# Optimization experiments

Hardware: AMD Instinct MI355X
Metric: run time of the kernel (lower is better)

The kernel has to match this reference:

```python
import jax, jax.numpy as jnp
import numpy as np

B, IN_DIM, OUT_DIM, DEGREE = 512, 256, 256, 5
SCALE = 0.5 / (DEGREE + 1)


def setup_inputs() -> dict:
    key = jax.random.key(0)
    k1, k2, k3 = jax.random.split(key, 3)
    x = jax.random.normal(k1, (B, IN_DIM), dtype=jnp.float32)
    slopes = jnp.arange(DEGREE + 1, dtype=jnp.float32)
    weights_p = jax.random.normal(k2, (IN_DIM, OUT_DIM, DEGREE + 1), dtype=jnp.float32) * SCALE
    weights_q = jax.random.normal(k3, (IN_DIM, OUT_DIM, DEGREE + 1), dtype=jnp.float32) * SCALE
    return {"x": x, "slopes": slopes, "weights_p": weights_p, "weights_q": weights_q}


def reference(x, slopes, weights_p, weights_q):
    # Training-mode forward (temp = 1.0): logsumexp over degree axis.
    # lin: (B, in_dim, 1, degree+1)
    lin = x[:, :, None, None] * slopes
    # broadcast with (in_dim, out_dim, degree+1) -> (B, in_dim, out_dim, degree+1)
    p_val = jax.nn.logsumexp(lin + weights_p, axis=-1)  # (B, in_dim, out_dim)
    q_val = jax.nn.logsumexp(lin + weights_q, axis=-1)  # (B, in_dim, out_dim)
    return jnp.sum(p_val - q_val, axis=1)  # (B, out_dim)
```

## Files before the change

kernel.cpp:

```cpp
#include <hip/hip_runtime.h>
#include <math.h>

#define BATCH   512
#define IN_DIM  256
#define OUT_DIM 256
#define NDEG    6

#define OT     8
#define NSEG   32
#define ISEG   8
#define NB     8

typedef float v2f __attribute__((ext_vector_type(2)));

__device__ __forceinline__ v2f pk_fma_blo(v2f a, v2f t, v2f c) {
    v2f d;
    asm("v_pk_fma_f32 %0, %1, %2, %3 op_sel:[0,0,0] op_sel_hi:[1,0,1]"
        : "=v"(d) : "v"(a), "v"(t), "v"(c));
    return d;
}
__device__ __forceinline__ v2f pk_fma_bhi(v2f a, v2f t, v2f c) {
    v2f d;
    asm("v_pk_fma_f32 %0, %1, %2, %3 op_sel:[0,1,0] op_sel_hi:[1,1,1]"
        : "=v"(d) : "v"(a), "v"(t), "v"(c));
    return d;
}
__device__ __forceinline__ v2f pk_mul(v2f a, v2f b) {
    v2f d;
    asm("v_pk_mul_f32 %0, %1, %2" : "=v"(d) : "v"(a), "v"(b));
    return d;
}

#define PRESCALE 12.476649250079015f

__global__ void prep_pack(const float* __restrict__ wp,
                          const float* __restrict__ wq,
                          float4* __restrict__ pk2) {
    int j = blockIdx.x * blockDim.x + threadIdx.x;
    if (j >= IN_DIM * OUT_DIM) return;
    const int i = j >> 8, o = j & 255;
    const int seg_blk = i >> 6;
    const int seg     = (i >> 3) & 7;
    const int ii      = i & 7;
    const int o_blk   = o >> 3;
    const int o_l     = o & 7;
    const size_t base =
        ((size_t)(o_blk * 4 + seg_blk) * 24) * 64 + seg * 8 + o_l;

    const float2* wp2 = (const float2*)wp;
    const float2* wq2 = (const float2*)wq;
    float2 p0 = wp2[j * 3], p1 = wp2[j * 3 + 1], p2 = wp2[j * 3 + 2];
    float2 q0 = wq2[j * 3], q1 = wq2[j * 3 + 1], q2 = wq2[j * 3 + 2];
    pk2[base + (ii * 3 + 0) * 64] =
        make_float4(__expf(p0.x - PRESCALE), __expf(q0.x - PRESCALE),
                    __expf(p0.y - PRESCALE), __expf(q0.y - PRESCALE));
    pk2[base + (ii * 3 + 1) * 64] =
        make_float4(__expf(p1.x - PRESCALE), __expf(q1.x - PRESCALE),
                    __expf(p1.y - PRESCALE), __expf(q1.y - PRESCALE));
    pk2[base + (ii * 3 + 2) * 64] =
        make_float4(__expf(p2.x - PRESCALE), __expf(q2.x - PRESCALE),
                    __expf(p2.y - PRESCALE), __expf(q2.y - PRESCALE));
}

__device__ __forceinline__ v2f horner_lo(float4 c0, float4 c1, float4 c2, v2f tp) {
    const v2f C0 = {c0.x, c0.y}, C1 = {c0.z, c0.w};
    const v2f C2 = {c1.x, c1.y}, C3 = {c1.z, c1.w};
    const v2f C4 = {c2.x, c2.y}, C5 = {c2.z, c2.w};
    v2f r = pk_fma_blo(C5, tp, C4);
    r = pk_fma_blo(r, tp, C3);
    r = pk_fma_blo(r, tp, C2);
    r = pk_fma_blo(r, tp, C1);
    r = pk_fma_blo(r, tp, C0);
    return r;
}
__device__ __forceinline__ v2f horner_hi(float4 c0, float4 c1, float4 c2, v2f tp) {
    const v2f C0 = {c0.x, c0.y}, C1 = {c0.z, c0.w};
    const v2f C2 = {c1.x, c1.y}, C3 = {c1.z, c1.w};
    const v2f C4 = {c2.x, c2.y}, C5 = {c2.z, c2.w};
    v2f r = pk_fma_bhi(C5, tp, C4);
    r = pk_fma_bhi(r, tp, C3);
    r = pk_fma_bhi(r, tp, C2);
    r = pk_fma_bhi(r, tp, C1);
    r = pk_fma_bhi(r, tp, C0);
    return r;
}

__launch_bounds__(256, 4)
__global__ void tropical_main(const float* __restrict__ x,
                              const float4* __restrict__ pk2,
                              float* __restrict__ out) {
    __shared__ float lds[NSEG * (NB * OT + 1)];

    const int tid = threadIdx.x;
    const int o_l = tid & (OT - 1);
    const int b0  = blockIdx.y * NB;

    {
        const int r = tid >> 5;
        const int c = (tid & 31) * 8;
        const float* xr = x + (size_t)(b0 + r) * IN_DIM + c;
        const float4 v0 = *(const float4*)(xr);
        const float4 v1 = *(const float4*)(xr + 4);
        float4 w0, w1;
        w0.x = __expf(v0.x); w0.y = __expf(v0.y);
        w0.z = __expf(v0.z); w0.w = __expf(v0.w);
        w1.x = __expf(v1.x); w1.y = __expf(v1.y);
        w1.z = __expf(v1.z); w1.w = __expf(v1.w);
        *(float4*)&lds[r * IN_DIM + c]     = w0;
        *(float4*)&lds[r * IN_DIM + c + 4] = w1;
    }
    __syncthreads();

    float acc[NB];
#pragma unroll
    for (int b = 0; b < NB; ++b) acc[b] = 0.f;

    const int lane = tid & 63;
    const int wv   = tid >> 6;
    const float4* __restrict__ cb =
        pk2 + ((size_t)(blockIdx.x * 4 + wv) * 24) * 64 + lane;

    const int i0 = (tid >> 3) * ISEG;
    const float* __restrict__ tb = lds + i0;

#pragma unroll
    for (int g = 0; g < 2; ++g) {
        float4 C[12];
#pragma unroll
        for (int k = 0; k < 12; ++k)
            C[k] = cb[(g * 12 + k) * 64];

#pragma unroll
        for (int b = 0; b < NB; ++b) {
            const float4 tv = *(const float4*)(tb + b * IN_DIM + g * 4);
            const v2f txy = {tv.x, tv.y};
            const v2f tzw = {tv.z, tv.w};
            const v2f PQ0 = horner_lo(C[0], C[1],  C[2],  txy);
            const v2f PQ1 = horner_hi(C[3], C[4],  C[5],  txy);
            const v2f PQ2 = horner_lo(C[6], C[7],  C[8],  tzw);
            const v2f PQ3 = horner_hi(C[9], C[10], C[11], tzw);
            const v2f m = pk_mul(pk_mul(PQ0, PQ1), pk_mul(PQ2, PQ3));
            acc[b] += __log2f(m.x) - __log2f(m.y);
        }
    }

    __syncthreads();
    const int seg = tid >> 3;
#pragma unroll
    for (int b = 0; b < NB; ++b)
        lds[seg * (NB * OT + 1) + b * OT + o_l] = acc[b];
    __syncthreads();

    if (tid < NB * OT) {
        const int br = tid >> 3, orr = tid & (OT - 1);
        float s = 0.f;
#pragma unroll
        for (int g = 0; g < NSEG; ++g)
            s += lds[g * (NB * OT + 1) + br * OT + orr];
        out[(size_t)(b0 + br) * OUT_DIM + blockIdx.x * OT + orr] =
            s * 0.6931471805599453f;
    }
}

__global__ void tropical_fallback(const float* __restrict__ x,
                                  const float* __restrict__ wp,
                                  const float* __restrict__ wq,
                                  float* __restrict__ out) {
    const int o = blockIdx.x * 16 + (threadIdx.x & 15);
    const int b = blockIdx.y * 16 + (threadIdx.x >> 4);
    float acc = 0.f;
    for (int i = 0; i < IN_DIM; ++i) {
        const float xv = x[b * IN_DIM + i];
        const float* p = wp + (size_t)(i * OUT_DIM + o) * NDEG;
        const float* q = wq + (size_t)(i * OUT_DIM + o) * NDEG;
        float lp[NDEG], lq[NDEG], mP = -1e30f, mQ = -1e30f;
#pragma unroll
        for (int d = 0; d < NDEG; ++d) {
            lp[d] = xv * d + p[d]; mP = fmaxf(mP, lp[d]);
            lq[d] = xv * d + q[d]; mQ = fmaxf(mQ, lq[d]);
        }
        float sP = 0.f, sQ = 0.f;
#pragma unroll
        for (int d = 0; d < NDEG; ++d) {
            sP += __expf(lp[d] - mP);
            sQ += __expf(lq[d] - mQ);
        }
        acc += (mP + __logf(sP)) - (mQ + __logf(sQ));
    }
    out[b * OUT_DIM + o] = acc;
}

extern "C" void kernel_launch(void* const* d_in, const int* in_sizes, int n_in,
                              void* d_out, int out_size, void* d_ws, size_t ws_size,
                              hipStream_t stream) {
    const float* x  = (const float*)d_in[0];
    const float* wp = (const float*)d_in[2];
    const float* wq = (const float*)d_in[3];
    float* out = (float*)d_out;

    const size_t pk_bytes = (size_t)IN_DIM * OUT_DIM * 12 * sizeof(float);

    if (ws_size >= pk_bytes) {
        float4* pk2 = (float4*)d_ws;
        prep_pack<<<(IN_DIM * OUT_DIM + 255) / 256, 256, 0, stream>>>(wp, wq, pk2);

        dim3 grid(OUT_DIM / OT, BATCH / NB);
        tropical_main<<<grid, 256, 0, stream>>>(x, (const float4*)pk2, out);
    } else {
        dim3 grid(OUT_DIM / 16, BATCH / 16);
        tropical_fallback<<<grid, 256, 0, stream>>>(x, wp, wq, out);
    }
}
```

Measured before the change: 23.30 us.

## Precompute exp(x) in fused prep kernel and parallelize final segment reduction

The weight-packing kernel now also computes exp(x) for the whole batch into a workspace buffer, using extra blocks, and its weight blocks are remapped so each block covers an output slice across a chunk of inputs. The main kernel loads the precomputed exp(x) instead of recomputing it, which removes the 32-fold redundant exponentials done per output block. The final reduction over 32 segments is split into a two-stage tree using all threads, replacing a serial loop run by 64 threads. The cost is a larger workspace requirement and an extra global round-trip for the exp(x) values.

```diff
diff --git a/kernel.cpp b/kernel.cpp
--- a/kernel.cpp
+++ b/kernel.cpp
@@ -33,33 +33,46 @@
 
 #define PRESCALE 12.476649250079015f
 
-__global__ void prep_pack(const float* __restrict__ wp,
-                          const float* __restrict__ wq,
-                          float4* __restrict__ pk2) {
-    int j = blockIdx.x * blockDim.x + threadIdx.x;
-    if (j >= IN_DIM * OUT_DIM) return;
-    const int i = j >> 8, o = j & 255;
-    const int seg_blk = i >> 6;
-    const int seg     = (i >> 3) & 7;
-    const int ii      = i & 7;
-    const int o_blk   = o >> 3;
-    const int o_l     = o & 7;
-    const size_t base =
-        ((size_t)(o_blk * 4 + seg_blk) * 24) * 64 + seg * 8 + o_l;
-
-    const float2* wp2 = (const float2*)wp;
-    const float2* wq2 = (const float2*)wq;
-    float2 p0 = wp2[j * 3], p1 = wp2[j * 3 + 1], p2 = wp2[j * 3 + 2];
-    float2 q0 = wq2[j * 3], q1 = wq2[j * 3 + 1], q2 = wq2[j * 3 + 2];
-    pk2[base + (ii * 3 + 0) * 64] =
-        make_float4(__expf(p0.x - PRESCALE), __expf(q0.x - PRESCALE),
-                    __expf(p0.y - PRESCALE), __expf(q0.y - PRESCALE));
-    pk2[base + (ii * 3 + 1) * 64] =
-        make_float4(__expf(p1.x - PRESCALE), __expf(q1.x - PRESCALE),
-                    __expf(p1.y - PRESCALE), __expf(q1.y - PRESCALE));
-    pk2[base + (ii * 3 + 2) * 64] =
-        make_float4(__expf(p2.x - PRESCALE), __expf(q2.x - PRESCALE),
-                    __expf(p2.y - PRESCALE), __expf(q2.y - PRESCALE));
+__global__ void prep_fused(const float* __restrict__ x,
+                           const float* __restrict__ wp,
+                           const float* __restrict__ wq,
+                           float4* __restrict__ pk2,
+                           float4* __restrict__ texp4) {
+    const int p   = blockIdx.x;
+    const int tid = threadIdx.x;
+    if (p < 256) {
+        const int ob  = p & 31;
+        const int ch  = p >> 5;
+        const int i   = ch * 32 + (tid >> 3);
+        const int o_l = tid & 7;
+        const int o   = ob * 8 + o_l;
+        const int j   = i * OUT_DIM + o;
+
+        const int seg_blk = i >> 6;
+        const int seg     = (i >> 3) & 7;
+        const int ii      = i & 7;
+        const size_t base =
+            ((size_t)(ob * 4 + seg_blk) * 24) * 64 + seg * 8 + o_l;
+
+        const float2* wp2 = (const float2*)wp;
+        const float2* wq2 = (const float2*)wq;
+        float2 p0 = wp2[j * 3], p1 = wp2[j * 3 + 1], p2 = wp2[j * 3 + 2];
+        float2 q0 = wq2[j * 3], q1 = wq2[j * 3 + 1], q2 = wq2[j * 3 + 2];
+        pk2[base + (ii * 3 + 0) * 64] =
+            make_float4(__expf(p0.x - PRESCALE), __expf(q0.x - PRESCALE),
+                        __expf(p0.y - PRESCALE), __expf(q0.y - PRESCALE));
+        pk2[base + (ii * 3 + 1) * 64] =
+            make_float4(__expf(p1.x - PRESCALE), __expf(q1.x - PRESCALE),
+                        __expf(p1.y - PRESCALE), __expf(q1.y - PRESCALE));
+        pk2[base + (ii * 3 + 2) * 64] =
+            make_float4(__expf(p2.x - PRESCALE), __expf(q2.x - PRESCALE),
+                        __expf(p2.y - PRESCALE), __expf(q2.y - PRESCALE));
+    } else {
+        const int idx = (p - 256) * 256 + tid;
+        const float4 v = ((const float4*)x)[idx];
+        texp4[idx] = make_float4(__expf(v.x), __expf(v.y),
+                                 __expf(v.z), __expf(v.w));
+    }
 }
 
 __device__ __forceinline__ v2f horner_lo(float4 c0, float4 c1, float4 c2, v2f tp) {
@@ -86,10 +99,10 @@
 }
 
 __launch_bounds__(256, 4)
-__global__ void tropical_main(const float* __restrict__ x,
+__global__ void tropical_main(const float4* __restrict__ texp4,
                               const float4* __restrict__ pk2,
                               float* __restrict__ out) {
-    __shared__ float lds[NSEG * (NB * OT + 1)];
+    __shared__ float lds[NSEG * (NB * OT + 1) + 256];
 
     const int tid = threadIdx.x;
     const int o_l = tid & (OT - 1);
@@ -98,16 +111,11 @@
     {
         const int r = tid >> 5;
         const int c = (tid & 31) * 8;
-        const float* xr = x + (size_t)(b0 + r) * IN_DIM + c;
-        const float4 v0 = *(const float4*)(xr);
-        const float4 v1 = *(const float4*)(xr + 4);
-        float4 w0, w1;
-        w0.x = __expf(v0.x); w0.y = __expf(v0.y);
-        w0.z = __expf(v0.z); w0.w = __expf(v0.w);
-        w1.x = __expf(v1.x); w1.y = __expf(v1.y);
-        w1.z = __expf(v1.z); w1.w = __expf(v1.w);
-        *(float4*)&lds[r * IN_DIM + c]     = w0;
-        *(float4*)&lds[r * IN_DIM + c + 4] = w1;
+        const float4* tx = texp4 + ((size_t)(b0 + r) * IN_DIM + c) / 4;
+        const float4 v0 = tx[0];
+        const float4 v1 = tx[1];
+        *(float4*)&lds[r * IN_DIM + c]     = v0;
+        *(float4*)&lds[r * IN_DIM + c + 4] = v1;
     }
     __syncthreads();
 
@@ -151,12 +159,23 @@
         lds[seg * (NB * OT + 1) + b * OT + o_l] = acc[b];
     __syncthreads();
 
+    {
+        const int outI = tid >> 2;
+        const int quad = tid & 3;
+        const int br   = outI >> 3;
+        const int orr  = outI & 7;
+        float s = 0.f;
+#pragma unroll
+        for (int g2 = 0; g2 < 8; ++g2)
+            s += lds[(quad * 8 + g2) * (NB * OT + 1) + br * OT + orr];
+        lds[NSEG * (NB * OT + 1) + outI * 4 + quad] = s;
+    }
+    __syncthreads();
+
     if (tid < NB * OT) {
-        const int br = tid >> 3, orr = tid & (OT - 1);
-        float s = 0.f;
-#pragma unroll
-        for (int g = 0; g < NSEG; ++g)
-            s += lds[g * (NB * OT + 1) + br * OT + orr];
+        const float* pr = lds + NSEG * (NB * OT + 1) + tid * 4;
+        const float s = (pr[0] + pr[1]) + (pr[2] + pr[3]);
+        const int br = tid >> 3, orr = tid & 7;
         out[(size_t)(b0 + br) * OUT_DIM + blockIdx.x * OT + orr] =
             s * 0.6931471805599453f;
     }
@@ -198,14 +217,17 @@
     const float* wq = (const float*)d_in[3];
     float* out = (float*)d_out;
 
-    const size_t pk_bytes = (size_t)IN_DIM * OUT_DIM * 12 * sizeof(float);
-
-    if (ws_size >= pk_bytes) {
-        float4* pk2 = (float4*)d_ws;
-        prep_pack<<<(IN_DIM * OUT_DIM + 255) / 256, 256, 0, stream>>>(wp, wq, pk2);
+    const size_t pk_bytes   = (size_t)IN_DIM * OUT_DIM * 12 * sizeof(float);
+    const size_t texp_bytes = (size_t)BATCH * IN_DIM * sizeof(float);
+
+    if (ws_size >= pk_bytes + texp_bytes) {
+        float4* pk2   = (float4*)d_ws;
+        float4* texp4 = (float4*)((char*)d_ws + pk_bytes);
+
+        prep_fused<<<384, 256, 0, stream>>>(x, wp, wq, pk2, texp4);
 
         dim3 grid(OUT_DIM / OT, BATCH / NB);
-        tropical_main<<<grid, 256, 0, stream>>>(x, (const float4*)pk2, out);
+        tropical_main<<<grid, 256, 0, stream>>>(texp4, (const float4*)pk2, out);
     } else {
         dim3 grid(OUT_DIM / 16, BATCH / 16);
         tropical_fallback<<<grid, 256, 0, stream>>>(x, wp, wq, out);
```

New measurement: 23.14 us. No clear change (-0.7%).

## Fuse weight exp-packing into main kernel and parallelize final reduction

Applied to the files above, without the earlier changes.

Removes the separate prep kernel and workspace buffer; each block now loads raw p/q weights and computes their exponentials inline before the Horner evaluation. The final cross-segment reduction is split into a two-stage reduction using all threads. This avoids a launch and the packed-buffer write/read, but recomputes the weight exponentials once per batch tile and uses less coalesced loads.

```diff
diff --git a/kernel.cpp b/kernel.cpp
--- a/kernel.cpp
+++ b/kernel.cpp
@@ -4,7 +4,6 @@
 #define BATCH   512
 #define IN_DIM  256
 #define OUT_DIM 256
-#define NDEG    6
 
 #define OT     8
 #define NSEG   32
@@ -33,35 +32,6 @@
 
 #define PRESCALE 12.476649250079015f
 
-__global__ void prep_pack(const float* __restrict__ wp,
-                          const float* __restrict__ wq,
-                          float4* __restrict__ pk2) {
-    int j = blockIdx.x * blockDim.x + threadIdx.x;
-    if (j >= IN_DIM * OUT_DIM) return;
-    const int i = j >> 8, o = j & 255;
-    const int seg_blk = i >> 6;
-    const int seg     = (i >> 3) & 7;
-    const int ii      = i & 7;
-    const int o_blk   = o >> 3;
-    const int o_l     = o & 7;
-    const size_t base =
-        ((size_t)(o_blk * 4 + seg_blk) * 24) * 64 + seg * 8 + o_l;
-
-    const float2* wp2 = (const float2*)wp;
-    const float2* wq2 = (const float2*)wq;
-    float2 p0 = wp2[j * 3], p1 = wp2[j * 3 + 1], p2 = wp2[j * 3 + 2];
-    float2 q0 = wq2[j * 3], q1 = wq2[j * 3 + 1], q2 = wq2[j * 3 + 2];
-    pk2[base + (ii * 3 + 0) * 64] =
-        make_float4(__expf(p0.x - PRESCALE), __expf(q0.x - PRESCALE),
-                    __expf(p0.y - PRESCALE), __expf(q0.y - PRESCALE));
-    pk2[base + (ii * 3 + 1) * 64] =
-        make_float4(__expf(p1.x - PRESCALE), __expf(q1.x - PRESCALE),
-                    __expf(p1.y - PRESCALE), __expf(q1.y - PRESCALE));
-    pk2[base + (ii * 3 + 2) * 64] =
-        make_float4(__expf(p2.x - PRESCALE), __expf(q2.x - PRESCALE),
-                    __expf(p2.y - PRESCALE), __expf(q2.y - PRESCALE));
-}
-
 __device__ __forceinline__ v2f horner_lo(float4 c0, float4 c1, float4 c2, v2f tp) {
     const v2f C0 = {c0.x, c0.y}, C1 = {c0.z, c0.w};
     const v2f C2 = {c1.x, c1.y}, C3 = {c1.z, c1.w};
@@ -86,10 +56,11 @@
 }
 
 __launch_bounds__(256, 4)
-__global__ void tropical_main(const float* __restrict__ x,
-                              const float4* __restrict__ pk2,
-                              float* __restrict__ out) {
-    __shared__ float lds[NSEG * (NB * OT + 1)];
+__global__ void tropical_fused(const float* __restrict__ x,
+                               const float* __restrict__ wp,
+                               const float* __restrict__ wq,
+                               float* __restrict__ out) {
+    __shared__ float lds[NSEG * (NB * OT + 1) + 256];
 
     const int tid = threadIdx.x;
     const int o_l = tid & (OT - 1);
@@ -115,20 +86,31 @@
 #pragma unroll
     for (int b = 0; b < NB; ++b) acc[b] = 0.f;
 
-    const int lane = tid & 63;
-    const int wv   = tid >> 6;
-    const float4* __restrict__ cb =
-        pk2 + ((size_t)(blockIdx.x * 4 + wv) * 24) * 64 + lane;
-
-    const int i0 = (tid >> 3) * ISEG;
-    const float* __restrict__ tb = lds + i0;
+    const int seg    = tid >> 3;
+    const int i_base = seg * ISEG;
+    const int o      = blockIdx.x * OT + o_l;
+    const float* __restrict__ tb = lds + i_base;
 
 #pragma unroll
     for (int g = 0; g < 2; ++g) {
         float4 C[12];
 #pragma unroll
-        for (int k = 0; k < 12; ++k)
-            C[k] = cb[(g * 12 + k) * 64];
+        for (int ii = 0; ii < 4; ++ii) {
+            const int j = (i_base + g * 4 + ii) * OUT_DIM + o;
+            const float2* P2 = (const float2*)wp + (size_t)j * 3;
+            const float2* Q2 = (const float2*)wq + (size_t)j * 3;
+            const float2 p0 = P2[0], p1 = P2[1], p2 = P2[2];
+            const float2 q0 = Q2[0], q1 = Q2[1], q2 = Q2[2];
+            C[ii * 3 + 0] = make_float4(
+                __expf(p0.x - PRESCALE), __expf(q0.x - PRESCALE),
+                __expf(p0.y - PRESCALE), __expf(q0.y - PRESCALE));
+            C[ii * 3 + 1] = make_float4(
+                __expf(p1.x - PRESCALE), __expf(q1.x - PRESCALE),
+                __expf(p1.y - PRESCALE), __expf(q1.y - PRESCALE));
+            C[ii * 3 + 2] = make_float4(
+                __expf(p2.x - PRESCALE), __expf(q2.x - PRESCALE),
+                __expf(p2.y - PRESCALE), __expf(q2.y - PRESCALE));
+        }
 
 #pragma unroll
         for (int b = 0; b < NB; ++b) {
@@ -145,49 +127,31 @@
     }
 
     __syncthreads();
-    const int seg = tid >> 3;
 #pragma unroll
     for (int b = 0; b < NB; ++b)
         lds[seg * (NB * OT + 1) + b * OT + o_l] = acc[b];
     __syncthreads();
 
-    if (tid < NB * OT) {
-        const int br = tid >> 3, orr = tid & (OT - 1);
+    {
+        const int outI = tid >> 2;
+        const int quad = tid & 3;
+        const int br   = outI >> 3;
+        const int orr  = outI & 7;
         float s = 0.f;
 #pragma unroll
-        for (int g = 0; g < NSEG; ++g)
-            s += lds[g * (NB * OT + 1) + br * OT + orr];
+        for (int g2 = 0; g2 < 8; ++g2)
+            s += lds[(quad * 8 + g2) * (NB * OT + 1) + br * OT + orr];
+        lds[NSEG * (NB * OT + 1) + outI * 4 + quad] = s;
+    }
+    __syncthreads();
+
+    if (tid < NB * OT) {
+        const float* pr = lds + NSEG * (NB * OT + 1) + tid * 4;
+        const float s = (pr[0] + pr[1]) + (pr[2] + pr[3]);
+        const int br = tid >> 3, orr = tid & 7;
         out[(size_t)(b0 + br) * OUT_DIM + blockIdx.x * OT + orr] =
             s * 0.6931471805599453f;
     }
-}
-
-__global__ void tropical_fallback(const float* __restrict__ x,
-                                  const float* __restrict__ wp,
-                                  const float* __restrict__ wq,
-                                  float* __restrict__ out) {
-    const int o = blockIdx.x * 16 + (threadIdx.x & 15);
-    const int b = blockIdx.y * 16 + (threadIdx.x >> 4);
-    float acc = 0.f;
-    for (int i = 0; i < IN_DIM; ++i) {
-        const float xv = x[b * IN_DIM + i];
-        const float* p = wp + (size_t)(i * OUT_DIM + o) * NDEG;
-        const float* q = wq + (size_t)(i * OUT_DIM + o) * NDEG;
-        float lp[NDEG], lq[NDEG], mP = -1e30f, mQ = -1e30f;
-#pragma unroll
-        for (int d = 0; d < NDEG; ++d) {
-            lp[d] = xv * d + p[d]; mP = fmaxf(mP, lp[d]);
-            lq[d] = xv * d + q[d]; mQ = fmaxf(mQ, lq[d]);
-        }
-        float sP = 0.f, sQ = 0.f;
-#pragma unroll
-        for (int d = 0; d < NDEG; ++d) {
-            sP += __expf(lp[d] - mP);
-            sQ += __expf(lq[d] - mQ);
-        }
-        acc += (mP + __logf(sP)) - (mQ + __logf(sQ));
-    }
-    out[b * OUT_DIM + o] = acc;
 }
 
 extern "C" void kernel_launch(void* const* d_in, const int* in_sizes, int n_in,
@@ -198,16 +162,6 @@
     const float* wq = (const float*)d_in[3];
     float* out = (float*)d_out;
 
-    const size_t pk_bytes = (size_t)IN_DIM * OUT_DIM * 12 * sizeof(float);
-
-    if (ws_size >= pk_bytes) {
-        float4* pk2 = (float4*)d_ws;
-        prep_pack<<<(IN_DIM * OUT_DIM + 255) / 256, 256, 0, stream>>>(wp, wq, pk2);
-
-        dim3 grid(OUT_DIM / OT, BATCH / NB);
-        tropical_main<<<grid, 256, 0, stream>>>(x, (const float4*)pk2, out);
-    } else {
-        dim3 grid(OUT_DIM / 16, BATCH / 16);
-        tropical_fallback<<<grid, 256, 0, stream>>>(x, wp, wq, out);
-    }
+    dim3 grid(OUT_DIM / OT, BATCH / NB);
+    tropical_fused<<<grid, 256, 0, stream>>>(x, wp, wq, out);
 }
```

Result: faster. 22.23 us (-4.6%).
